# Kernel tuning notes

Hardware: AMD Instinct MI355X
Metric: run time of the kernel (lower is better)

Reference implementation:

```python
import jax, jax.numpy as jnp
import numpy as np

CHUNK = 128      # chunk_size
NUM_BITS = 6     # log2(num_experts=64)


def setup_inputs() -> dict:
    key = jax.random.key(0)
    k1, k2, k3 = jax.random.split(key, 3)
    B, L, D, E = 4, 4096, 1024, 64
    x = jax.random.normal(k1, (B, L, D), dtype=jnp.float32)
    expert_weights = jax.random.normal(k2, (E, D, D), dtype=jnp.float32) * 0.02
    hyperplanes = jax.random.normal(k3, (D, NUM_BITS), dtype=jnp.float32)
    return {"x": x, "expert_weights": expert_weights, "hyperplanes": hyperplanes}


def reference(x, expert_weights, hyperplanes):
    # x: [B, L, D]; L divisible by CHUNK (no padding path taken)
    B, L, D = x.shape
    C = L // CHUNK
    xr = x.reshape(B, C, CHUNK, D)

    # --- LSH (SimHash) router, chunk-level ---
    chunk_emb = xr.mean(axis=2)                      # [B, C, D]
    proj = chunk_emb @ hyperplanes                   # [B, C, bits]
    bits = (proj > 0).astype(jnp.int32)
    powers = (2 ** jnp.arange(NUM_BITS)).astype(jnp.int32)
    e1 = jnp.sum(bits * powers, axis=-1)             # [B, C]
    weakest = jnp.argmin(jnp.abs(proj), axis=-1)     # weakest hyperplane bit
    flip = (2 ** weakest).astype(jnp.int32)
    e2 = jnp.bitwise_xor(e1, flip)                   # second expert: flip weakest bit
    # gates are all 1.0 and router_threshold=0.0 -> confidence_mask = 1.0

    # --- per-chunk expert weight gather + bmm combine (top-2 average) ---
    out = jnp.zeros_like(xr)
    for idx in (e1, e2):
        w = expert_weights[idx]                      # [B, C, D, D] gathered
        out = out + jnp.einsum('bcld,bcde->bcle', xr, w)
    out = out * 0.5
    # dropout p=0.0 / eval -> identity
    return out.reshape(B, L, D)
```

## Files before the change

kernel.cpp:

```cpp
#include <hip/hip_runtime.h>
#include <hip/hip_bf16.h>


#define BD 4
#define LD 4096
#define DD 1024
#define ED 64
#define CHUNKD 128
#define NBITS 6
#define NCHUNK 128

typedef __bf16 bf16_8 __attribute__((ext_vector_type(8)));
typedef __bf16 bf16_4 __attribute__((ext_vector_type(4)));
typedef float floatx4 __attribute__((ext_vector_type(4)));

#define WT_PER_ENT  131072

__global__ __launch_bounds__(256) void sum_cvt_kernel(
    const float* __restrict__ x, __bf16* __restrict__ a, double* __restrict__ csum)
{
    const int chunk = blockIdx.x >> 3;
    const int tg = blockIdx.x & 7;
    const size_t base = (size_t)chunk * CHUNKD * DD + (size_t)tg * 16 * DD;
    const float* xc = x + base;
    __bf16* ac = a + base;
    const int t = threadIdx.x;

    double s0 = 0, s1 = 0, s2 = 0, s3 = 0;
    #pragma unroll 4
    for (int tok = 0; tok < 16; ++tok) {
        const float4 v = *(const float4*)(xc + tok * DD + t * 4);
        bf16_4 o;
        o[0] = (__bf16)v.x; o[1] = (__bf16)v.y; o[2] = (__bf16)v.z; o[3] = (__bf16)v.w;
        *(bf16_4*)(ac + tok * DD + t * 4) = o;
        s0 += (double)v.x; s1 += (double)v.y; s2 += (double)v.z; s3 += (double)v.w;
    }
    double* c = csum + (size_t)chunk * DD + t * 4;
    atomicAdd(c + 0, s0); atomicAdd(c + 1, s1);
    atomicAdd(c + 2, s2); atomicAdd(c + 3, s3);
}

__global__ __launch_bounds__(256) void router2_kernel(
    const double* __restrict__ csum, const float* __restrict__ hyp,
    int* __restrict__ eidx)
{
    const int chunk = blockIdx.x;
    const int t = threadIdx.x;
    double pj[NBITS];
    #pragma unroll
    for (int j = 0; j < NBITS; ++j) pj[j] = 0.0;
    #pragma unroll
    for (int i = 0; i < 4; ++i) {
        const int d = t + i * 256;
        const double emb = csum[(size_t)chunk * DD + d] * (1.0 / 128.0);
        #pragma unroll
        for (int j = 0; j < NBITS; ++j)
            pj[j] += emb * (double)hyp[d * NBITS + j];
    }
    #pragma unroll
    for (int off = 32; off > 0; off >>= 1) {
        #pragma unroll
        for (int j = 0; j < NBITS; ++j)
            pj[j] += __shfl_down(pj[j], off, 64);
    }
    __shared__ double red[4][NBITS];
    const int wave = t >> 6, lane = t & 63;
    if (lane == 0) {
        #pragma unroll
        for (int j = 0; j < NBITS; ++j) red[wave][j] = pj[j];
    }
    __syncthreads();
    if (t == 0) {
        int e1 = 0, weakest = 0;
        double best = 1e300;
        #pragma unroll
        for (int j = 0; j < NBITS; ++j) {
            double p = red[0][j] + red[1][j] + red[2][j] + red[3][j];
            if (p > 0.0) e1 |= (1 << j);
            double aa = fabs(p);
            if (aa < best) { best = aa; weakest = j; }
        }
        eidx[chunk * 2 + 0] = e1;
        eidx[chunk * 2 + 1] = e1 ^ (1 << weakest);
    }
}

__global__ __launch_bounds__(256) void wcvt_kernel(
    const float* __restrict__ W, __bf16* __restrict__ WtSw)
{
    __shared__ float tile[32 * 129];

    const int bx = blockIdx.x;
    const int kh = bx & 1;
    const int nt = (bx >> 1) & 7;
    const int e  = bx >> 4;
    const int t = threadIdx.x;

    const float* We = W + (size_t)e * DD * DD + nt * 128;
    __bf16* base_ent = WtSw + (size_t)(e * 8 + nt) * WT_PER_ENT;

    for (int it = 0; it < 16; ++it) {
        const int k0 = kh * 512 + it * 32;
        const int s  = kh * 16 + it;
        #pragma unroll
        for (int p = 0; p < 4; ++p) {
            const int idx = p * 256 + t;
            const int kr  = idx >> 5;
            const int nc4 = idx & 31;
            const float4 v = *(const float4*)(We + (size_t)(k0 + kr) * DD + nc4 * 4);
            float* dst = &tile[kr * 129 + nc4 * 4];
            dst[0] = v.x; dst[1] = v.y; dst[2] = v.z; dst[3] = v.w;
        }
        __syncthreads();
        #pragma unroll
        for (int c = 0; c < 2; ++c) {
            const int cell = c * 256 + t;
            const int l  = cell & 63;
            const int rb = cell >> 6;
            const int q  = l >> 4;
            const int lr = l & 15;
            bf16_8 o;
            #pragma unroll
            for (int j = 0; j < 8; ++j)
                o[j] = (__bf16)tile[(q * 8 + j) * 129 + rb * 16 + lr];
            *(bf16_8*)(base_ent + ((size_t)s * 8 + rb) * 512 + l * 8) = o;
        }
        __syncthreads();
    }
}

__global__ __launch_bounds__(256) void ffn_gemm_bf16(
    const __bf16* __restrict__ Abf,
    const __bf16* __restrict__ WtSw,
    const int* __restrict__ eidx,
    float* __restrict__ out)
{
    __shared__ __bf16 Als[8 * 512];
    __shared__ __bf16 B0ls[8 * 512];
    __shared__ __bf16 B1ls[8 * 512];

    const int bx = blockIdx.x;
    const int chunk = bx >> 3;
    const int ntb = bx & 7;
    const int t = threadIdx.x;
    const int lane = t & 63;
    const int wave = t >> 6;
    const int wm = wave >> 1;
    const int wn = wave & 1;
    const int lr = lane & 15;
    const int q  = lane >> 4;

    const int e0 = eidx[chunk * 2 + 0];
    const int e1 = eidx[chunk * 2 + 1];

    const __bf16* Ag = Abf + (size_t)chunk * CHUNKD * DD;
    const __bf16* Bg0 = WtSw + (size_t)(e0 * 8 + ntb) * WT_PER_ENT + lane * 8;
    const __bf16* Bg1 = WtSw + (size_t)(e1 * 8 + ntb) * WT_PER_ENT + lane * 8;

    const int rb0 = wave * 2;
    const __bf16* AgW0 = Ag + (size_t)(rb0 * 16 + lr) * DD + q * 8;
    const __bf16* AgW1 = Ag + (size_t)((rb0 + 1) * 16 + lr) * DD + q * 8;

    floatx4 acc[4][4] = {};

    for (int ks = 0; ks < 32; ++ks) {
        const int k0 = ks * 32;
        __builtin_amdgcn_global_load_lds(
            (const __attribute__((address_space(1))) void*)(AgW0 + k0),
            (__attribute__((address_space(3))) void*)(&Als[rb0 * 512]), 16, 0, 0);
        __builtin_amdgcn_global_load_lds(
            (const __attribute__((address_space(1))) void*)(AgW1 + k0),
            (__attribute__((address_space(3))) void*)(&Als[(rb0 + 1) * 512]), 16, 0, 0);
        #pragma unroll
        for (int i = 0; i < 2; ++i) {
            const int rb = rb0 + i;
            __builtin_amdgcn_global_load_lds(
                (const __attribute__((address_space(1))) void*)(Bg0 + ((size_t)ks * 8 + rb) * 512),
                (__attribute__((address_space(3))) void*)(&B0ls[rb * 512]), 16, 0, 0);
            __builtin_amdgcn_global_load_lds(
                (const __attribute__((address_space(1))) void*)(Bg1 + ((size_t)ks * 8 + rb) * 512),
                (__attribute__((address_space(3))) void*)(&B1ls[rb * 512]), 16, 0, 0);
        }
        __syncthreads();

        bf16_8 af[4], bb[4];
        #pragma unroll
        for (int mt = 0; mt < 4; ++mt)
            af[mt] = *(const bf16_8*)(&Als[(wm * 4 + mt) * 512 + lane * 8]);
        #pragma unroll
        for (int nt = 0; nt < 4; ++nt)
            bb[nt] = *(const bf16_8*)(&B0ls[(wn * 4 + nt) * 512 + lane * 8]);
        #pragma unroll
        for (int mt = 0; mt < 4; ++mt) {
            #pragma unroll
            for (int nt = 0; nt < 4; ++nt)
                acc[mt][nt] = __builtin_amdgcn_mfma_f32_16x16x32_bf16(
                    af[mt], bb[nt], acc[mt][nt], 0, 0, 0);
        }
        #pragma unroll
        for (int nt = 0; nt < 4; ++nt)
            bb[nt] = *(const bf16_8*)(&B1ls[(wn * 4 + nt) * 512 + lane * 8]);
        #pragma unroll
        for (int mt = 0; mt < 4; ++mt) {
            #pragma unroll
            for (int nt = 0; nt < 4; ++nt)
                acc[mt][nt] = __builtin_amdgcn_mfma_f32_16x16x32_bf16(
                    af[mt], bb[nt], acc[mt][nt], 0, 0, 0);
        }
        __syncthreads();
    }

    const size_t orow0 = (size_t)chunk * CHUNKD;
    const int n0 = ntb * 128;
    #pragma unroll
    for (int mt = 0; mt < 4; ++mt) {
        #pragma unroll
        for (int nt = 0; nt < 4; ++nt) {
            const int col = n0 + wn * 64 + nt * 16 + lr;
            #pragma unroll
            for (int r = 0; r < 4; ++r) {
                const int row = wm * 64 + mt * 16 + q * 4 + r;
                out[(orow0 + row) * DD + col] = acc[mt][nt][r] * 0.5f;
            }
        }
    }
}

__global__ __launch_bounds__(256) void router_kernel(
    const float* __restrict__ x, const float* __restrict__ hyp,
    int* __restrict__ eidx)
{
    const int chunk = blockIdx.x;
    const int t = threadIdx.x;
    const float* xc = x + (size_t)chunk * CHUNKD * DD;
    double cs[4] = {0.0, 0.0, 0.0, 0.0};
    for (int tok = 0; tok < CHUNKD; ++tok) {
        const float* row = xc + tok * DD;
        #pragma unroll
        for (int i = 0; i < 4; ++i) cs[i] += (double)row[t + i * 256];
    }
    double pj[NBITS];
    #pragma unroll
    for (int j = 0; j < NBITS; ++j) pj[j] = 0.0;
    #pragma unroll
    for (int i = 0; i < 4; ++i) {
        const int d = t + i * 256;
        const double emb = cs[i] * (1.0 / 128.0);
        #pragma unroll
        for (int j = 0; j < NBITS; ++j) pj[j] += emb * (double)hyp[d * NBITS + j];
    }
    #pragma unroll
    for (int off = 32; off > 0; off >>= 1) {
        #pragma unroll
        for (int j = 0; j < NBITS; ++j) pj[j] += __shfl_down(pj[j], off, 64);
    }
    __shared__ double red[4][NBITS];
    const int wave = t >> 6, lane = t & 63;
    if (lane == 0) {
        #pragma unroll
        for (int j = 0; j < NBITS; ++j) red[wave][j] = pj[j];
    }
    __syncthreads();
    if (t == 0) {
        int e1 = 0, weakest = 0;
        double best = 1e300;
        #pragma unroll
        for (int j = 0; j < NBITS; ++j) {
            double p = red[0][j] + red[1][j] + red[2][j] + red[3][j];
            if (p > 0.0) e1 |= (1 << j);
            double a = fabs(p);
            if (a < best) { best = a; weakest = j; }
        }
        eidx[chunk * 2 + 0] = e1;
        eidx[chunk * 2 + 1] = e1 ^ (1 << weakest);
    }
}

__global__ __launch_bounds__(256) void cvt_x_kernel(
    const float* __restrict__ x, __bf16* __restrict__ a)
{
    const size_t i = ((size_t)blockIdx.x * 256 + threadIdx.x) * 4;
    const float4 v = *(const float4*)(x + i);
    bf16_4 o;
    o[0] = (__bf16)v.x; o[1] = (__bf16)v.y; o[2] = (__bf16)v.z; o[3] = (__bf16)v.w;
    *(bf16_4*)(a + i) = o;
}

__global__ __launch_bounds__(256) void ffn_gemm_fp32w(
    const __bf16* __restrict__ Abf, const float* __restrict__ W,
    const int* __restrict__ eidx, float* __restrict__ out)
{
    __shared__ __bf16 Als[128 * 32];
    __shared__ __bf16 Bls[128 * 32];
    const int bx = blockIdx.x;
    const int chunk = bx >> 3;
    const int n0 = (bx & 7) * 128;
    const int t = threadIdx.x;
    const int lane = t & 63;
    const int wave = t >> 6;
    const int wm = wave >> 1;
    const int wn = wave & 1;
    const int lr = lane & 15;
    const int q  = lane >> 4;
    const int ee[2] = {eidx[chunk * 2 + 0], eidx[chunk * 2 + 1]};
    const __bf16* Ag = Abf + (size_t)chunk * CHUNKD * DD;
    const int a_col = (lane & 3) * 8;
    const int a_rsub = lane >> 2;
    floatx4 acc[4][4] = {};
    for (int xp = 0; xp < 2; ++xp) {
        const float* We = W + (size_t)ee[xp] * (DD * DD) + n0;
        for (int k0 = 0; k0 < DD; k0 += 32) {
            float bv[2][8];
            #pragma unroll
            for (int rep = 0; rep < 2; ++rep) {
                const int nb = wave * 16 + lr + rep * 64;
                const float* src = We + (size_t)(k0 + q * 8) * DD + nb;
                #pragma unroll
                for (int j = 0; j < 8; ++j) bv[rep][j] = src[(size_t)j * DD];
            }
            #pragma unroll
            for (int i = 0; i < 2; ++i) {
                const __bf16* ga = Ag + (size_t)((wave * 2 + i) * 16 + a_rsub) * DD + k0 + a_col;
                __builtin_amdgcn_global_load_lds(
                    (const __attribute__((address_space(1))) void*)ga,
                    (__attribute__((address_space(3))) void*)(&Als[(wave * 2 + i) * 512]),
                    16, 0, 0);
            }
            #pragma unroll
            for (int rep = 0; rep < 2; ++rep) {
                const int nb = wave * 16 + lr + rep * 64;
                bf16_8 bw;
                #pragma unroll
                for (int j = 0; j < 8; ++j) bw[j] = (__bf16)bv[rep][j];
                *(bf16_8*)(&Bls[nb * 32 + q * 8]) = bw;
            }
            __syncthreads();
            bf16_8 af[4], bfr[4];
            #pragma unroll
            for (int mt = 0; mt < 4; ++mt)
                af[mt] = *(const bf16_8*)(&Als[(wm * 64 + mt * 16 + lr) * 32 + q * 8]);
            #pragma unroll
            for (int nt = 0; nt < 4; ++nt)
                bfr[nt] = *(const bf16_8*)(&Bls[(wn * 64 + nt * 16 + lr) * 32 + q * 8]);
            #pragma unroll
            for (int mt = 0; mt < 4; ++mt) {
                #pragma unroll
                for (int nt = 0; nt < 4; ++nt)
                    acc[mt][nt] = __builtin_amdgcn_mfma_f32_16x16x32_bf16(
                        af[mt], bfr[nt], acc[mt][nt], 0, 0, 0);
            }
            __syncthreads();
        }
    }
    const size_t orow0 = (size_t)chunk * CHUNKD;
    #pragma unroll
    for (int mt = 0; mt < 4; ++mt) {
        #pragma unroll
        for (int nt = 0; nt < 4; ++nt) {
            const int col = n0 + wn * 64 + nt * 16 + lr;
            #pragma unroll
            for (int r = 0; r < 4; ++r) {
                const int row = wm * 64 + mt * 16 + q * 4 + r;
                out[(orow0 + row) * DD + col] = acc[mt][nt][r] * 0.5f;
            }
        }
    }
}

extern "C" void kernel_launch(void* const* d_in, const int* in_sizes, int n_in,
                              void* d_out, int out_size, void* d_ws, size_t ws_size,
                              hipStream_t stream) {
    const float* x   = (const float*)d_in[0];
    const float* W   = (const float*)d_in[1];
    const float* hyp = (const float*)d_in[2];
    float* out = (float*)d_out;

    const size_t off_eidx = 0;
    const size_t off_csum = 4096;
    const size_t off_a    = off_csum + (size_t)NCHUNK * DD * 8;
    const size_t off_wt   = off_a + (size_t)NCHUNK * CHUNKD * DD * 2;
    const size_t need     = off_wt + (size_t)ED * DD * DD * 2;

    int* eidx = (int*)((char*)d_ws + off_eidx);
    __bf16* Abf = (__bf16*)((char*)d_ws + off_a);

    if (ws_size >= need) {
        double* csum = (double*)((char*)d_ws + off_csum);
        __bf16* WtSw = (__bf16*)((char*)d_ws + off_wt);
        hipMemsetAsync(csum, 0, (size_t)NCHUNK * DD * 8, stream);
        sum_cvt_kernel<<<NCHUNK * 8, 256, 0, stream>>>(x, Abf, csum);
        wcvt_kernel<<<ED * 16, 256, 0, stream>>>(W, WtSw);
        router2_kernel<<<NCHUNK, 256, 0, stream>>>(csum, hyp, eidx);
        ffn_gemm_bf16<<<NCHUNK * 8, 256, 0, stream>>>(Abf, WtSw, eidx, out);
    } else {
        __bf16* Abf2 = (__bf16*)((char*)d_ws + 1024);
        router_kernel<<<NCHUNK, 256, 0, stream>>>(x, hyp, eidx);
        cvt_x_kernel<<<(BD * LD * DD) / (256 * 4), 256, 0, stream>>>(x, Abf2);
        ffn_gemm_fp32w<<<NCHUNK * 8, 256, 0, stream>>>(Abf2, W, eidx, out);
    }
}
```

Measured before the change: 541.2 us.

## Skip conversion of unused experts and drop atomics for chunk sums

The router now runs before the weight conversion kernel, and the conversion skips any expert not selected by some chunk. Because eidx holds 256 entries, each of the 256 threads checks exactly one. Chunk sums are written as per-subgroup partials instead of double atomics, which removes the memset, and the router reduces the 8 partials itself. The goal is to cut atomic contention and avoid converting expert weights that no chunk uses, at the cost of a larger partial-sum buffer and an extra dependency between router and conversion.

```diff
diff --git a/kernel.cpp b/kernel.cpp
--- a/kernel.cpp
+++ b/kernel.cpp
@@ -17,7 +17,7 @@
 #define WT_PER_ENT  131072
 
 __global__ __launch_bounds__(256) void sum_cvt_kernel(
-    const float* __restrict__ x, __bf16* __restrict__ a, double* __restrict__ csum)
+    const float* __restrict__ x, __bf16* __restrict__ a, double* __restrict__ csum_p)
 {
     const int chunk = blockIdx.x >> 3;
     const int tg = blockIdx.x & 7;
@@ -35,13 +35,12 @@
         *(bf16_4*)(ac + tok * DD + t * 4) = o;
         s0 += (double)v.x; s1 += (double)v.y; s2 += (double)v.z; s3 += (double)v.w;
     }
-    double* c = csum + (size_t)chunk * DD + t * 4;
-    atomicAdd(c + 0, s0); atomicAdd(c + 1, s1);
-    atomicAdd(c + 2, s2); atomicAdd(c + 3, s3);
+    double* c = csum_p + ((size_t)(chunk * 8 + tg)) * DD + t * 4;
+    c[0] = s0; c[1] = s1; c[2] = s2; c[3] = s3;
 }
 
 __global__ __launch_bounds__(256) void router2_kernel(
-    const double* __restrict__ csum, const float* __restrict__ hyp,
+    const double* __restrict__ csum_p, const float* __restrict__ hyp,
     int* __restrict__ eidx)
 {
     const int chunk = blockIdx.x;
@@ -52,7 +51,11 @@
     #pragma unroll
     for (int i = 0; i < 4; ++i) {
         const int d = t + i * 256;
-        const double emb = csum[(size_t)chunk * DD + d] * (1.0 / 128.0);
+        double cs = 0.0;
+        #pragma unroll
+        for (int tg = 0; tg < 8; ++tg)
+            cs += csum_p[((size_t)(chunk * 8 + tg)) * DD + d];
+        const double emb = cs * (1.0 / 128.0);
         #pragma unroll
         for (int j = 0; j < NBITS; ++j)
             pj[j] += emb * (double)hyp[d * NBITS + j];
@@ -86,15 +89,23 @@
 }
 
 __global__ __launch_bounds__(256) void wcvt_kernel(
-    const float* __restrict__ W, __bf16* __restrict__ WtSw)
+    const float* __restrict__ W, __bf16* __restrict__ WtSw,
+    const int* __restrict__ eidx)
 {
     __shared__ float tile[32 * 129];
+    __shared__ int s_used;
 
     const int bx = blockIdx.x;
     const int kh = bx & 1;
     const int nt = (bx >> 1) & 7;
     const int e  = bx >> 4;
     const int t = threadIdx.x;
+
+    if (t == 0) s_used = 0;
+    __syncthreads();
+    if (eidx[t] == e) s_used = 1;
+    __syncthreads();
+    if (!s_used) return;
 
     const float* We = W + (size_t)e * DD * DD + nt * 128;
     __bf16* base_ent = WtSw + (size_t)(e * 8 + nt) * WT_PER_ENT;
@@ -377,7 +388,7 @@
 
     const size_t off_eidx = 0;
     const size_t off_csum = 4096;
-    const size_t off_a    = off_csum + (size_t)NCHUNK * DD * 8;
+    const size_t off_a    = off_csum + (size_t)NCHUNK * 8 * DD * 8;
     const size_t off_wt   = off_a + (size_t)NCHUNK * CHUNKD * DD * 2;
     const size_t need     = off_wt + (size_t)ED * DD * DD * 2;
 
@@ -385,12 +396,11 @@
     __bf16* Abf = (__bf16*)((char*)d_ws + off_a);
 
     if (ws_size >= need) {
-        double* csum = (double*)((char*)d_ws + off_csum);
+        double* csum_p = (double*)((char*)d_ws + off_csum);
         __bf16* WtSw = (__bf16*)((char*)d_ws + off_wt);
-        hipMemsetAsync(csum, 0, (size_t)NCHUNK * DD * 8, stream);
-        sum_cvt_kernel<<<NCHUNK * 8, 256, 0, stream>>>(x, Abf, csum);
-        wcvt_kernel<<<ED * 16, 256, 0, stream>>>(W, WtSw);
-        router2_kernel<<<NCHUNK, 256, 0, stream>>>(csum, hyp, eidx);
+        sum_cvt_kernel<<<NCHUNK * 8, 256, 0, stream>>>(x, Abf, csum_p);
+        router2_kernel<<<NCHUNK, 256, 0, stream>>>(csum_p, hyp, eidx);
+        wcvt_kernel<<<ED * 16, 256, 0, stream>>>(W, WtSw, eidx);
         ffn_gemm_bf16<<<NCHUNK * 8, 256, 0, stream>>>(Abf, WtSw, eidx, out);
     } else {
         __bf16* Abf2 = (__bf16*)((char*)d_ws + 1024);
```

Result: no change. 531.0 us (-1.9%).
